# Kernel optimization log

Measured on AMD Instinct MI355X. Metric: run time of the kernel, lower is better.

The kernel has to match this reference:

```python
import jax, jax.numpy as jnp
import numpy as np

B, T, C, H, NIN = 4, 16384, 512, 8, 2
D = C // H


def setup_inputs() -> dict:
    key = jax.random.key(0)
    ks = jax.random.split(key, 12)
    s = 1.0 / np.sqrt(C)
    return {
        "x1": jax.random.normal(ks[0], (B, T, C), jnp.float32),
        "x2": jax.random.normal(ks[1], (B, T, C), jnp.float32),
        "y0": jax.random.normal(ks[2], (B, T, C), jnp.float32),
        "y1": jax.random.normal(ks[3], (B, T, C), jnp.float32),
        "Wq": jax.random.normal(ks[4], (C, C), jnp.float32) * s,
        "bq": jnp.zeros((C,), jnp.float32),
        "Wk": jax.random.normal(ks[5], (C, C), jnp.float32) * s,
        "bk": jnp.zeros((C,), jnp.float32),
        "Wv": jax.random.normal(ks[6], (NIN, C, C), jnp.float32) * s,
        "bv": jnp.zeros((NIN, C), jnp.float32),
        "Wp": jax.random.normal(ks[7], (C, C), jnp.float32) * s,
        "bp": jnp.zeros((C,), jnp.float32),
    }


def _heads(x):
    # [B, T, C] -> [B, H, T, D]
    b, t, c = x.shape
    return x.reshape(b, t, H, D).transpose(0, 2, 1, 3)


def reference(x1, x2, y0, y1, Wq, bq, Wk, bk, Wv, bv, Wp, bp):
    # q, k: softmax feature maps over head dim
    q = jax.nn.softmax(_heads(x1 @ Wq + bq), axis=-1)  # [B,H,T1,D]
    k = jax.nn.softmax(_heads(x2 @ Wk + bk), axis=-1)  # [B,H,T2,D]
    # v = sum of per-input value projections
    ys = jnp.stack([y0, y1], axis=0)  # [NIN,B,T2,C]
    v = jnp.einsum('ibtc,icd->btd', ys, Wv) + bv.sum(axis=0)
    v = _heads(v)  # [B,H,T2,D]
    # linear attention: k^T v then q @ (kv)
    k_v = jnp.einsum('bhtd,bhte->bhde', k, v)      # [B,H,D,D]
    q_k_v = jnp.einsum('bhsd,bhde->bhse', q, k_v)  # [B,H,T1,D]
    k_cumsum = k.sum(axis=-2, keepdims=True)       # [B,H,1,D]
    D_inv = 1.0 / (q * k_cumsum).sum(axis=-1, keepdims=True)
    out = q_k_v * D_inv                            # [B,H,T1,D]
    out = out.transpose(0, 2, 1, 3).reshape(x1.shape[0], x1.shape[1], C)
    return out @ Wp + bp
```

## Files before the change

### kernel.cpp

```cpp
#include <hip/hip_runtime.h>
#include <cstdint>
#include <cstddef>

#define BB 4
#define TT 16384
#define CC 512
#define HH 8
#define DD 64
#define MTOT (BB*TT)

typedef __attribute__((ext_vector_type(4))) float f32x4;
typedef __bf16 bf16;
typedef __attribute__((ext_vector_type(8))) bf16 bf16x8;
typedef __attribute__((ext_vector_type(4))) bf16 bf16x4;

static __device__ __forceinline__ float b2f(bf16 x) { return (float)x; }
static __device__ __forceinline__ bf16  f2b(float x) { return (bf16)x; }

static __device__ __forceinline__ void gload16(const bf16* src, bf16* ldsbase) {
    __builtin_amdgcn_global_load_lds(
        (const __attribute__((address_space(1))) void*)src,
        (__attribute__((address_space(3))) void*)ldsbase, 16, 0, 0);
}

__global__ __launch_bounds__(256) void transpose_w5(
    const float* __restrict__ W0, const float* __restrict__ W1,
    const float* __restrict__ W2, const float* __restrict__ W3,
    const float* __restrict__ W4,
    bf16* __restrict__ T0, bf16* __restrict__ T1, bf16* __restrict__ T2,
    bf16* __restrict__ T3, bf16* __restrict__ T4)
{
    __shared__ float tile[32][33];
    const int which = blockIdx.x >> 8;
    const float* W = which == 0 ? W0 : which == 1 ? W1 : which == 2 ? W2
                   : which == 3 ? W3 : W4;
    bf16* Wt = which == 0 ? T0 : which == 1 ? T1 : which == 2 ? T2
             : which == 3 ? T3 : T4;
    const int t = blockIdx.x & 255;
    const int r0 = (t >> 4) * 32, c0 = (t & 15) * 32;
    const int tid = threadIdx.x;
    {
        int r = tid >> 3, c4 = (tid & 7) << 2;
        float4 v = *(const float4*)(W + (size_t)(r0 + r) * 512 + c0 + c4);
        tile[r][c4 + 0] = v.x; tile[r][c4 + 1] = v.y;
        tile[r][c4 + 2] = v.z; tile[r][c4 + 3] = v.w;
    }
    __syncthreads();
    {
        int n = tid >> 3, k4 = (tid & 7) << 2;
        bf16x4 o;
        o[0] = f2b(tile[k4 + 0][n]); o[1] = f2b(tile[k4 + 1][n]);
        o[2] = f2b(tile[k4 + 2][n]); o[3] = f2b(tile[k4 + 3][n]);
        *(bf16x4*)(Wt + (size_t)(c0 + n) * 512 + r0 + k4) = o;
    }
}

template<int MODE>
__global__ __launch_bounds__(512) void gemm_proj(
    const float* A0, const float* A1, const bf16* Abf,
    const bf16* Wt0, const bf16* Wt1,
    const float* bias0, const float* bias1,
    bf16* outb, float* outf, int m_base)
{
    constexpr int KSTEPS = (MODE == 2) ? 16 : 8;
    __shared__ bf16 Asm[128 * 72];
    __shared__ bf16 Bsm[2][512 * 64];

    const int tid = threadIdx.x;
    const int lane = tid & 63;
    const int w = tid >> 6;
    const int l15 = lane & 15, lg = lane >> 4;
    const size_t m0 = (size_t)(blockIdx.x + m_base) * 128;

    const int arow = tid >> 2, ac16 = (tid & 3) << 4;
    const int blr = lane >> 3;
    const int bsc = ((lane & 7) ^ blr) << 3;

    f32x4 acc[8][4];
#pragma unroll
    for (int m = 0; m < 8; ++m)
#pragma unroll
        for (int n = 0; n < 4; ++n) acc[m][n] = (f32x4){0.f, 0.f, 0.f, 0.f};

    float4 apf[4];
    bf16x8 apb[2];

    auto issueA = [&](int t) {
        if (MODE == 3) {
#pragma unroll
            for (int j = 0; j < 2; ++j)
                apb[j] = *(const bf16x8*)(Abf + (m0 + arow) * CC + (t & 7) * 64
                                          + ac16 + j * 8);
        } else {
            const float* Af = (MODE == 2 && t >= 8) ? A1 : A0;
#pragma unroll
            for (int j = 0; j < 4; ++j)
                apf[j] = *(const float4*)(Af + (m0 + arow) * CC + (t & 7) * 64
                                          + ac16 + j * 4);
        }
    };
    auto writeA = [&]() {
        if (MODE == 3) {
#pragma unroll
            for (int j = 0; j < 2; ++j)
                *(bf16x8*)&Asm[arow * 72 + ac16 + j * 8] = apb[j];
        } else {
#pragma unroll
            for (int j = 0; j < 4; ++j) {
                bf16x4 s;
                s[0] = f2b(apf[j].x); s[1] = f2b(apf[j].y);
                s[2] = f2b(apf[j].z); s[3] = f2b(apf[j].w);
                *(bf16x4*)&Asm[arow * 72 + ac16 + j * 4] = s;
            }
        }
    };
    auto issueB = [&](int t, int buf) {
        const bf16* Wt = (MODE == 2 && t >= 8) ? Wt1 : Wt0;
#pragma unroll
        for (int g = 0; g < 8; ++g) {
            int rowbase = w * 64 + g * 8;
            gload16(Wt + (size_t)(rowbase + blr) * CC + (t & 7) * 64 + bsc,
                    &Bsm[buf][rowbase * 64]);
        }
    };

    issueA(0);
    issueB(0, 0);
    writeA();
    asm volatile("s_waitcnt lgkmcnt(0)" ::: "memory");

    int cur = 0;
    for (int ko = 0; ko < KSTEPS; ++ko) {
        const bool more = ko + 1 < KSTEPS;
        if (more) { issueA(ko + 1); issueB(ko + 1, cur ^ 1); }
        if (more) {
            if (MODE == 3) asm volatile("s_waitcnt vmcnt(10)" ::: "memory");
            else           asm volatile("s_waitcnt vmcnt(12)" ::: "memory");
        } else {
            asm volatile("s_waitcnt vmcnt(0)" ::: "memory");
        }
        __builtin_amdgcn_s_barrier();
        bf16x8 af[8][2], bfv[4][2];
#pragma unroll
        for (int m = 0; m < 8; ++m)
#pragma unroll
            for (int kk = 0; kk < 2; ++kk)
                af[m][kk] = *(const bf16x8*)&Asm[(m * 16 + l15) * 72 + kk * 32 + lg * 8];
#pragma unroll
        for (int n = 0; n < 4; ++n) {
            int row = w * 64 + n * 16 + l15;
            int swz = (l15 & 7) << 3;
#pragma unroll
            for (int kk = 0; kk < 2; ++kk)
                bfv[n][kk] = *(const bf16x8*)&Bsm[cur][row * 64
                                                      + ((kk * 32 + lg * 8) ^ swz)];
        }
#pragma unroll
        for (int kk = 0; kk < 2; ++kk)
#pragma unroll
            for (int m = 0; m < 8; ++m)
#pragma unroll
                for (int n = 0; n < 4; ++n)
                    acc[m][n] = __builtin_amdgcn_mfma_f32_16x16x32_bf16(
                        af[m][kk], bfv[n][kk], acc[m][n], 0, 0, 0);
        __builtin_amdgcn_s_barrier();
        if (more) {
            writeA();
            asm volatile("s_waitcnt lgkmcnt(0)" ::: "memory");
        }
        cur ^= 1;
    }

    float bias[4];
#pragma unroll
    for (int n = 0; n < 4; ++n) {
        int col = w * 64 + n * 16 + l15;
        float bvv = bias0 ? bias0[col] : 0.f;
        if (MODE == 2) bvv += bias1[col];
        bias[n] = bvv;
    }
#pragma unroll
    for (int m = 0; m < 8; ++m) {
#pragma unroll
        for (int reg = 0; reg < 4; ++reg) {
            int r = m * 16 + lg * 4 + reg;
            float v0 = acc[m][0][reg] + bias[0];
            float v1 = acc[m][1][reg] + bias[1];
            float v2 = acc[m][2][reg] + bias[2];
            float v3 = acc[m][3][reg] + bias[3];
            if (MODE == 0) {
                float mx = fmaxf(fmaxf(v0, v1), fmaxf(v2, v3));
#pragma unroll
                for (int s = 1; s < 16; s <<= 1) mx = fmaxf(mx, __shfl_xor(mx, s, 64));
                v0 = __expf(v0 - mx); v1 = __expf(v1 - mx);
                v2 = __expf(v2 - mx); v3 = __expf(v3 - mx);
                float sm = v0 + v1 + v2 + v3;
#pragma unroll
                for (int s = 1; s < 16; s <<= 1) sm += __shfl_xor(sm, s, 64);
                float inv = 1.0f / sm;
                v0 *= inv; v1 *= inv; v2 *= inv; v3 *= inv;
            }
            size_t rowoff = (m0 + r) * CC + w * 64 + l15;
            if (MODE == 3) {
                outf[rowoff + 0]  = v0; outf[rowoff + 16] = v1;
                outf[rowoff + 32] = v2; outf[rowoff + 48] = v3;
            } else {
                outb[rowoff + 0]  = f2b(v0); outb[rowoff + 16] = f2b(v1);
                outb[rowoff + 32] = f2b(v2); outb[rowoff + 48] = f2b(v3);
            }
        }
    }
}

__global__ __launch_bounds__(256) void kv_partial2(
    const bf16* __restrict__ Kb, const bf16* __restrict__ Vb,
    float* __restrict__ part)
{
    __shared__ float Ks[32][68], Vs[32][68];
    const int tid = threadIdx.x;
    const int bh = blockIdx.x >> 5, chunk = blockIdx.x & 31;
    const int b = bh >> 3, h = bh & 7;
    const size_t base = (size_t)b * TT * CC + h * 64;
    const int d0 = (tid & 15) * 4, e0 = (tid >> 4) * 4;

    float acc[4][4];
#pragma unroll
    for (int i = 0; i < 4; ++i)
#pragma unroll
        for (int j = 0; j < 4; ++j) acc[i][j] = 0.f;
    float ks[4] = {0.f, 0.f, 0.f, 0.f};

    const int tstart = chunk * 512;
    for (int t0 = tstart; t0 < tstart + 512; t0 += 32) {
        __syncthreads();
#pragma unroll
        for (int rep = 0; rep < 2; ++rep) {
            int idx = (tid + rep * 256) * 4;
            int t = idx >> 6, dc = idx & 63;
            const bf16* gk = Kb + base + (size_t)(t0 + t) * CC + dc;
            const bf16* gv = Vb + base + (size_t)(t0 + t) * CC + dc;
            bf16x4 k4 = *(const bf16x4*)gk;
            bf16x4 v4 = *(const bf16x4*)gv;
            *(float4*)&Ks[t][dc] = make_float4(b2f(k4[0]), b2f(k4[1]), b2f(k4[2]), b2f(k4[3]));
            *(float4*)&Vs[t][dc] = make_float4(b2f(v4[0]), b2f(v4[1]), b2f(v4[2]), b2f(v4[3]));
        }
        __syncthreads();
#pragma unroll 8
        for (int tt = 0; tt < 32; ++tt) {
            float4 kf4 = *(const float4*)&Ks[tt][d0];
            float4 vf4 = *(const float4*)&Vs[tt][e0];
            if (e0 == 0) {
                ks[0] += kf4.x; ks[1] += kf4.y; ks[2] += kf4.z; ks[3] += kf4.w;
            }
            acc[0][0] += kf4.x * vf4.x; acc[0][1] += kf4.x * vf4.y;
            acc[0][2] += kf4.x * vf4.z; acc[0][3] += kf4.x * vf4.w;
            acc[1][0] += kf4.y * vf4.x; acc[1][1] += kf4.y * vf4.y;
            acc[1][2] += kf4.y * vf4.z; acc[1][3] += kf4.y * vf4.w;
            acc[2][0] += kf4.z * vf4.x; acc[2][1] += kf4.z * vf4.y;
            acc[2][2] += kf4.z * vf4.z; acc[2][3] += kf4.z * vf4.w;
            acc[3][0] += kf4.w * vf4.x; acc[3][1] += kf4.w * vf4.y;
            acc[3][2] += kf4.w * vf4.z; acc[3][3] += kf4.w * vf4.w;
        }
    }

    float* p = part + (size_t)blockIdx.x * 4160;
#pragma unroll
    for (int i = 0; i < 4; ++i)
#pragma unroll
        for (int j = 0; j < 4; ++j) p[(d0 + i) * 64 + (e0 + j)] = acc[i][j];
    if (tid < 16) {
#pragma unroll
        for (int i = 0; i < 4; ++i) p[4096 + d0 + i] = ks[i];
    }
}

__global__ __launch_bounds__(256) void kv_reduce(
    const float* __restrict__ part, float* __restrict__ kvT,
    float* __restrict__ ksum)
{
    const int bh = blockIdx.x >> 3, sl = blockIdx.x & 7;
    const int tid = threadIdx.x;
    const float* p0 = part + (size_t)bh * 32 * 4160;
    const int i0 = sl * 520, i1 = i0 + 520;
    for (int i = i0 + tid; i < i1; i += 256) {
        float s = 0.f;
        for (int c = 0; c < 32; ++c) s += p0[(size_t)c * 4160 + i];
        if (i < 4096) {
            int d = i >> 6, e = i & 63;
            kvT[(size_t)bh * 4096 + e * 64 + d] = s;
        } else {
            ksum[bh * 64 + (i - 4096)] = s;
        }
    }
}

__global__ __launch_bounds__(256) void qkv_norm2(
    bf16* Qb, const float* __restrict__ kvT, const float* __restrict__ ksum)
{
    __shared__ float Qs[64][68];
    __shared__ float KVs[64][68];
    __shared__ float ksm[8][64];
    const int tid = threadIdx.x;
    const size_t t0 = (size_t)blockIdx.x * 64;
    const int b = (int)(t0 / TT);
    const int rg = tid >> 4, cg = tid & 15;

    for (int i = tid; i < 512; i += 256) ksm[i >> 6][i & 63] = ksum[b * 512 + i];

    for (int h = 0; h < 8; ++h) {
        __syncthreads();
        const float* kvb = kvT + (size_t)(b * 8 + h) * 4096;
#pragma unroll
        for (int rep = 0; rep < 4; ++rep) {
            int idx = (tid + rep * 256) * 4;
            int rr = idx >> 6, dc = idx & 63;
            bf16x4 q4 = *(const bf16x4*)(Qb + (t0 + rr) * CC + h * 64 + dc);
            Qs[dc + 0][rr] = b2f(q4[0]); Qs[dc + 1][rr] = b2f(q4[1]);
            Qs[dc + 2][rr] = b2f(q4[2]); Qs[dc + 3][rr] = b2f(q4[3]);
            float4 v4 = *(const float4*)(kvb + rr * 64 + dc);
            KVs[dc + 0][rr] = v4.x; KVs[dc + 1][rr] = v4.y;
            KVs[dc + 2][rr] = v4.z; KVs[dc + 3][rr] = v4.w;
        }
        __syncthreads();

        float acc[4][4];
#pragma unroll
        for (int i = 0; i < 4; ++i)
#pragma unroll
            for (int j = 0; j < 4; ++j) acc[i][j] = 0.f;
        float dot[4] = {0.f, 0.f, 0.f, 0.f};

#pragma unroll 4
        for (int d = 0; d < 64; ++d) {
            float ksd = ksm[h][d];
            float4 kv4 = *(const float4*)&KVs[d][cg * 4];
            float4 q4 = *(const float4*)&Qs[d][rg * 4];
            dot[0] += q4.x * ksd; dot[1] += q4.y * ksd;
            dot[2] += q4.z * ksd; dot[3] += q4.w * ksd;
            acc[0][0] += q4.x * kv4.x; acc[0][1] += q4.x * kv4.y;
            acc[0][2] += q4.x * kv4.z; acc[0][3] += q4.x * kv4.w;
            acc[1][0] += q4.y * kv4.x; acc[1][1] += q4.y * kv4.y;
            acc[1][2] += q4.y * kv4.z; acc[1][3] += q4.y * kv4.w;
            acc[2][0] += q4.z * kv4.x; acc[2][1] += q4.z * kv4.y;
            acc[2][2] += q4.z * kv4.z; acc[2][3] += q4.z * kv4.w;
            acc[3][0] += q4.w * kv4.x; acc[3][1] += q4.w * kv4.y;
            acc[3][2] += q4.w * kv4.z; acc[3][3] += q4.w * kv4.w;
        }
#pragma unroll
        for (int i = 0; i < 4; ++i) {
            float dinv = 1.0f / dot[i];
            bf16x4 o;
#pragma unroll
            for (int j = 0; j < 4; ++j) o[j] = f2b(acc[i][j] * dinv);
            *(bf16x4*)(Qb + (t0 + rg * 4 + i) * CC + h * 64 + cg * 4) = o;
        }
    }
}

extern "C" void kernel_launch(void* const* d_in, const int* in_sizes, int n_in,
                              void* d_out, int out_size, void* d_ws, size_t ws_size,
                              hipStream_t stream)
{
    const float* x1 = (const float*)d_in[0];
    const float* x2 = (const float*)d_in[1];
    const float* y0 = (const float*)d_in[2];
    const float* y1 = (const float*)d_in[3];
    const float* Wq = (const float*)d_in[4];
    const float* bq = (const float*)d_in[5];
    const float* Wk = (const float*)d_in[6];
    const float* bk = (const float*)d_in[7];
    const float* Wv = (const float*)d_in[8];
    const float* bv = (const float*)d_in[9];
    const float* Wp = (const float*)d_in[10];
    const float* bp = (const float*)d_in[11];
    (void)in_sizes; (void)n_in; (void)out_size;

    char* ws = (char*)d_ws;
    size_t off = 0;
    auto alloc = [&](size_t bytes) -> void* {
        void* p = ws + off;
        off += (bytes + 255) & ~(size_t)255;
        return p;
    };
    bf16* WtQ  = (bf16*)alloc((size_t)512 * 512 * 2);
    bf16* WtK  = (bf16*)alloc((size_t)512 * 512 * 2);
    bf16* WtV0 = (bf16*)alloc((size_t)512 * 512 * 2);
    bf16* WtV1 = (bf16*)alloc((size_t)512 * 512 * 2);
    bf16* WtP  = (bf16*)alloc((size_t)512 * 512 * 2);
    float* ksum = (float*)alloc((size_t)32 * 64 * 4);
    float* kvT  = (float*)alloc((size_t)32 * 4096 * 4);
    float* part = (float*)alloc((size_t)1024 * 4160 * 4);
    bf16* Acopy = (bf16*)alloc((size_t)16 * 128 * CC * 2);

    const size_t QBYTES = (size_t)MTOT * CC * 2;
    bf16* Qb_ws = nullptr;
    if (ws_size >= off + QBYTES + 256) Qb_ws = (bf16*)alloc(QBYTES);

    bf16* Kb = (bf16*)d_out;
    bf16* Vb = Kb + (size_t)MTOT * CC;
    float* outF = (float*)d_out;

    transpose_w5<<<1280, 256, 0, stream>>>(Wq, Wk, Wv, Wv + (size_t)512 * 512, Wp,
                                           WtQ, WtK, WtV0, WtV1, WtP);

    gemm_proj<0><<<MTOT / 128, 512, 0, stream>>>(x2, nullptr, nullptr, WtK, nullptr,
                                                 bk, nullptr, Kb, nullptr, 0);
    gemm_proj<2><<<MTOT / 128, 512, 0, stream>>>(y0, y1, nullptr, WtV0, WtV1,
                                                 bv, bv + 512, Vb, nullptr, 0);
    kv_partial2<<<1024, 256, 0, stream>>>(Kb, Vb, part);
    kv_reduce<<<256, 256, 0, stream>>>(part, kvT, ksum);

    if (Qb_ws) {
        gemm_proj<0><<<MTOT / 128, 512, 0, stream>>>(x1, nullptr, nullptr, WtQ, nullptr,
                                                     bq, nullptr, Qb_ws, nullptr, 0);
        qkv_norm2<<<1024, 256, 0, stream>>>(Qb_ws, kvT, ksum);
        gemm_proj<3><<<MTOT / 128, 512, 0, stream>>>(nullptr, nullptr, (const bf16*)Qb_ws,
                                                     WtP, nullptr, bp, nullptr,
                                                     nullptr, outF, 0);
    } else {
        bf16* Qb = Kb;
        gemm_proj<0><<<MTOT / 128, 512, 0, stream>>>(x1, nullptr, nullptr, WtQ, nullptr,
                                                     bq, nullptr, Qb, nullptr, 0);
        qkv_norm2<<<1024, 256, 0, stream>>>(Qb, kvT, ksum);
        hipMemcpyAsync(Acopy, Qb, (size_t)16 * 128 * CC * 2, hipMemcpyDeviceToDevice,
                       stream);
        const int starts[5] = {256, 128, 64, 32, 16};
        const int counts[5] = {256, 128, 64, 32, 16};
        for (int p = 0; p < 5; ++p) {
            gemm_proj<3><<<counts[p], 512, 0, stream>>>(nullptr, nullptr, (const bf16*)Qb,
                                                        WtP, nullptr, bp, nullptr,
                                                        nullptr, outF, starts[p]);
        }
        gemm_proj<3><<<16, 512, 0, stream>>>(nullptr, nullptr, (const bf16*)Acopy,
                                             WtP, nullptr, bp, nullptr,
                                             nullptr, outF, 0);
    }
}
```

Baseline: 492.7 us.

## Fuse Q/K/V projection GEMMs into one launch and use MFMA for q·kv normalization

Merges the K, V and Q projection GEMMs into a single kernel that selects the projection by block index, removing launch gaps and tail idle time between them. Replaces the scalar LDS-based q@kv normalization kernel with an MFMA version that reads Q directly from global memory and converts kv to bf16. This adds precision loss from rounding kv to bf16, and the Q projection now runs alongside K/V rather than after the kv reduction.

```diff
diff --git a/kernel.cpp b/kernel.cpp
--- a/kernel.cpp
+++ b/kernel.cpp
@@ -56,21 +56,20 @@
 }
 
 template<int MODE>
-__global__ __launch_bounds__(512) void gemm_proj(
+static __device__ __forceinline__ void gemm_body(
     const float* A0, const float* A1, const bf16* Abf,
     const bf16* Wt0, const bf16* Wt1,
     const float* bias0, const float* bias1,
-    bf16* outb, float* outf, int m_base)
+    bf16* outb, float* outf, int bid,
+    bf16* Asm, bf16* BsmAll)
 {
     constexpr int KSTEPS = (MODE == 2) ? 16 : 8;
-    __shared__ bf16 Asm[128 * 72];
-    __shared__ bf16 Bsm[2][512 * 64];
 
     const int tid = threadIdx.x;
     const int lane = tid & 63;
     const int w = tid >> 6;
     const int l15 = lane & 15, lg = lane >> 4;
-    const size_t m0 = (size_t)(blockIdx.x + m_base) * 128;
+    const size_t m0 = (size_t)bid * 128;
 
     const int arow = tid >> 2, ac16 = (tid & 3) << 4;
     const int blr = lane >> 3;
@@ -116,11 +115,12 @@
     };
     auto issueB = [&](int t, int buf) {
         const bf16* Wt = (MODE == 2 && t >= 8) ? Wt1 : Wt0;
+        bf16* bb = BsmAll + buf * (512 * 64);
 #pragma unroll
         for (int g = 0; g < 8; ++g) {
             int rowbase = w * 64 + g * 8;
             gload16(Wt + (size_t)(rowbase + blr) * CC + (t & 7) * 64 + bsc,
-                    &Bsm[buf][rowbase * 64]);
+                    &bb[rowbase * 64]);
         }
     };
 
@@ -141,6 +141,7 @@
         }
         __builtin_amdgcn_s_barrier();
         bf16x8 af[8][2], bfv[4][2];
+        const bf16* bb = BsmAll + cur * (512 * 64);
 #pragma unroll
         for (int m = 0; m < 8; ++m)
 #pragma unroll
@@ -152,8 +153,7 @@
             int swz = (l15 & 7) << 3;
 #pragma unroll
             for (int kk = 0; kk < 2; ++kk)
-                bfv[n][kk] = *(const bf16x8*)&Bsm[cur][row * 64
-                                                      + ((kk * 32 + lg * 8) ^ swz)];
+                bfv[n][kk] = *(const bf16x8*)&bb[row * 64 + ((kk * 32 + lg * 8) ^ swz)];
         }
 #pragma unroll
         for (int kk = 0; kk < 2; ++kk)
@@ -210,6 +210,36 @@
             }
         }
     }
+}
+
+__global__ __launch_bounds__(512) void proj_fused(
+    const float* x1, const float* x2, const float* y0, const float* y1,
+    const bf16* WtQ, const bf16* WtK, const bf16* WtV0, const bf16* WtV1,
+    const float* bq, const float* bk, const float* bv0, const float* bv1,
+    bf16* Kb, bf16* Vb, bf16* Qb, int which_base)
+{
+    __shared__ bf16 Asm[128 * 72];
+    __shared__ bf16 Bsm[2 * 512 * 64];
+    const int which = which_base + ((int)blockIdx.x >> 9);
+    const int bid = blockIdx.x & 511;
+    if (which == 0)
+        gemm_body<0>(x2, nullptr, nullptr, WtK, nullptr, bk, nullptr,
+                     Kb, nullptr, bid, Asm, Bsm);
+    else if (which == 1)
+        gemm_body<2>(y0, y1, nullptr, WtV0, WtV1, bv0, bv1,
+                     Vb, nullptr, bid, Asm, Bsm);
+    else
+        gemm_body<0>(x1, nullptr, nullptr, WtQ, nullptr, bq, nullptr,
+                     Qb, nullptr, bid, Asm, Bsm);
+}
+
+__global__ __launch_bounds__(512) void gemm_proj3(
+    const bf16* Abf, const bf16* WtP, const float* bp, float* outf, int m_base)
+{
+    __shared__ bf16 Asm[128 * 72];
+    __shared__ bf16 Bsm[2 * 512 * 64];
+    gemm_body<3>(nullptr, nullptr, Abf, WtP, nullptr, bp, nullptr,
+                 nullptr, outf, blockIdx.x + m_base, Asm, Bsm);
 }
 
 __global__ __launch_bounds__(256) void kv_partial2(
@@ -294,66 +324,82 @@
     }
 }
 
-__global__ __launch_bounds__(256) void qkv_norm2(
-    bf16* Qb, const float* __restrict__ kvT, const float* __restrict__ ksum)
-{
-    __shared__ float Qs[64][68];
-    __shared__ float KVs[64][68];
+__global__ __launch_bounds__(256) void qkv_norm_mfma(
+    const bf16* Qb, const float* __restrict__ kvT,
+    const float* __restrict__ ksum, bf16* Ab)
+{
     __shared__ float ksm[8][64];
     const int tid = threadIdx.x;
+    const int lane = tid & 63;
+    const int w = tid >> 6;
+    const int l15 = lane & 15, lg = lane >> 4;
     const size_t t0 = (size_t)blockIdx.x * 64;
     const int b = (int)(t0 / TT);
-    const int rg = tid >> 4, cg = tid & 15;
 
     for (int i = tid; i < 512; i += 256) ksm[i >> 6][i & 63] = ksum[b * 512 + i];
-
-    for (int h = 0; h < 8; ++h) {
-        __syncthreads();
+    __syncthreads();
+
+#pragma unroll
+    for (int hi = 0; hi < 2; ++hi) {
+        const int h = w + hi * 4;
+        const bf16* qbase = Qb + t0 * CC + h * 64;
         const float* kvb = kvT + (size_t)(b * 8 + h) * 4096;
-#pragma unroll
-        for (int rep = 0; rep < 4; ++rep) {
-            int idx = (tid + rep * 256) * 4;
-            int rr = idx >> 6, dc = idx & 63;
-            bf16x4 q4 = *(const bf16x4*)(Qb + (t0 + rr) * CC + h * 64 + dc);
-            Qs[dc + 0][rr] = b2f(q4[0]); Qs[dc + 1][rr] = b2f(q4[1]);
-            Qs[dc + 2][rr] = b2f(q4[2]); Qs[dc + 3][rr] = b2f(q4[3]);
-            float4 v4 = *(const float4*)(kvb + rr * 64 + dc);
-            KVs[dc + 0][rr] = v4.x; KVs[dc + 1][rr] = v4.y;
-            KVs[dc + 2][rr] = v4.z; KVs[dc + 3][rr] = v4.w;
-        }
-        __syncthreads();
-
-        float acc[4][4];
-#pragma unroll
-        for (int i = 0; i < 4; ++i)
-#pragma unroll
-            for (int j = 0; j < 4; ++j) acc[i][j] = 0.f;
+
+        f32x4 acc[4][4];
+#pragma unroll
+        for (int m = 0; m < 4; ++m)
+#pragma unroll
+            for (int n = 0; n < 4; ++n) acc[m][n] = (f32x4){0.f, 0.f, 0.f, 0.f};
         float dot[4] = {0.f, 0.f, 0.f, 0.f};
 
-#pragma unroll 4
-        for (int d = 0; d < 64; ++d) {
-            float ksd = ksm[h][d];
-            float4 kv4 = *(const float4*)&KVs[d][cg * 4];
-            float4 q4 = *(const float4*)&Qs[d][rg * 4];
-            dot[0] += q4.x * ksd; dot[1] += q4.y * ksd;
-            dot[2] += q4.z * ksd; dot[3] += q4.w * ksd;
-            acc[0][0] += q4.x * kv4.x; acc[0][1] += q4.x * kv4.y;
-            acc[0][2] += q4.x * kv4.z; acc[0][3] += q4.x * kv4.w;
-            acc[1][0] += q4.y * kv4.x; acc[1][1] += q4.y * kv4.y;
-            acc[1][2] += q4.y * kv4.z; acc[1][3] += q4.y * kv4.w;
-            acc[2][0] += q4.z * kv4.x; acc[2][1] += q4.z * kv4.y;
-            acc[2][2] += q4.z * kv4.z; acc[2][3] += q4.z * kv4.w;
-            acc[3][0] += q4.w * kv4.x; acc[3][1] += q4.w * kv4.y;
-            acc[3][2] += q4.w * kv4.z; acc[3][3] += q4.w * kv4.w;
-        }
-#pragma unroll
-        for (int i = 0; i < 4; ++i) {
-            float dinv = 1.0f / dot[i];
-            bf16x4 o;
-#pragma unroll
-            for (int j = 0; j < 4; ++j) o[j] = f2b(acc[i][j] * dinv);
-            *(bf16x4*)(Qb + (t0 + rg * 4 + i) * CC + h * 64 + cg * 4) = o;
-        }
+#pragma unroll
+        for (int ks2 = 0; ks2 < 2; ++ks2) {
+            bf16x8 af[4], bfv[4];
+#pragma unroll
+            for (int m = 0; m < 4; ++m)
+                af[m] = *(const bf16x8*)(qbase + (size_t)(m * 16 + l15) * CC
+                                         + ks2 * 32 + lg * 8);
+#pragma unroll
+            for (int n = 0; n < 4; ++n) {
+                const float* kr = kvb + (n * 16 + l15) * 64 + ks2 * 32 + lg * 8;
+                float4 lo = *(const float4*)(kr + 0);
+                float4 hh = *(const float4*)(kr + 4);
+                bfv[n][0] = f2b(lo.x); bfv[n][1] = f2b(lo.y);
+                bfv[n][2] = f2b(lo.z); bfv[n][3] = f2b(lo.w);
+                bfv[n][4] = f2b(hh.x); bfv[n][5] = f2b(hh.y);
+                bfv[n][6] = f2b(hh.z); bfv[n][7] = f2b(hh.w);
+            }
+#pragma unroll
+            for (int m = 0; m < 4; ++m) {
+                float s = 0.f;
+#pragma unroll
+                for (int j = 0; j < 8; ++j)
+                    s += b2f(af[m][j]) * ksm[h][ks2 * 32 + lg * 8 + j];
+                dot[m] += s;
+            }
+#pragma unroll
+            for (int m = 0; m < 4; ++m)
+#pragma unroll
+                for (int n = 0; n < 4; ++n)
+                    acc[m][n] = __builtin_amdgcn_mfma_f32_16x16x32_bf16(
+                        af[m], bfv[n], acc[m][n], 0, 0, 0);
+        }
+#pragma unroll
+        for (int m = 0; m < 4; ++m) {
+            dot[m] += __shfl_xor(dot[m], 16, 64);
+            dot[m] += __shfl_xor(dot[m], 32, 64);
+        }
+#pragma unroll
+        for (int m = 0; m < 4; ++m)
+#pragma unroll
+            for (int reg = 0; reg < 4; ++reg) {
+                float dv = 1.0f / __shfl(dot[m], lg * 4 + reg, 64);
+                size_t ro = (t0 + m * 16 + lg * 4 + reg) * CC + h * 64 + l15;
+                Ab[ro + 0]  = f2b(acc[m][0][reg] * dv);
+                Ab[ro + 16] = f2b(acc[m][1][reg] * dv);
+                Ab[ro + 32] = f2b(acc[m][2][reg] * dv);
+                Ab[ro + 48] = f2b(acc[m][3][reg] * dv);
+            }
     }
 }
 
@@ -403,36 +449,34 @@
     transpose_w5<<<1280, 256, 0, stream>>>(Wq, Wk, Wv, Wv + (size_t)512 * 512, Wp,
                                            WtQ, WtK, WtV0, WtV1, WtP);
 
-    gemm_proj<0><<<MTOT / 128, 512, 0, stream>>>(x2, nullptr, nullptr, WtK, nullptr,
-                                                 bk, nullptr, Kb, nullptr, 0);
-    gemm_proj<2><<<MTOT / 128, 512, 0, stream>>>(y0, y1, nullptr, WtV0, WtV1,
-                                                 bv, bv + 512, Vb, nullptr, 0);
-    kv_partial2<<<1024, 256, 0, stream>>>(Kb, Vb, part);
-    kv_reduce<<<256, 256, 0, stream>>>(part, kvT, ksum);
-
     if (Qb_ws) {
-        gemm_proj<0><<<MTOT / 128, 512, 0, stream>>>(x1, nullptr, nullptr, WtQ, nullptr,
-                                                     bq, nullptr, Qb_ws, nullptr, 0);
-        qkv_norm2<<<1024, 256, 0, stream>>>(Qb_ws, kvT, ksum);
-        gemm_proj<3><<<MTOT / 128, 512, 0, stream>>>(nullptr, nullptr, (const bf16*)Qb_ws,
-                                                     WtP, nullptr, bp, nullptr,
-                                                     nullptr, outF, 0);
+        proj_fused<<<1536, 512, 0, stream>>>(x1, x2, y0, y1, WtQ, WtK, WtV0, WtV1,
+                                             bq, bk, bv, bv + 512,
+                                             Kb, Vb, Qb_ws, 0);
+        kv_partial2<<<1024, 256, 0, stream>>>(Kb, Vb, part);
+        kv_reduce<<<256, 256, 0, stream>>>(part, kvT, ksum);
+        qkv_norm_mfma<<<1024, 256, 0, stream>>>(Qb_ws, kvT, ksum, Qb_ws);
+        gemm_proj3<<<MTOT / 128, 512, 0, stream>>>((const bf16*)Qb_ws, WtP, bp,
+                                                   outF, 0);
     } else {
         bf16* Qb = Kb;
-        gemm_proj<0><<<MTOT / 128, 512, 0, stream>>>(x1, nullptr, nullptr, WtQ, nullptr,
-                                                     bq, nullptr, Qb, nullptr, 0);
-        qkv_norm2<<<1024, 256, 0, stream>>>(Qb, kvT, ksum);
+        proj_fused<<<1024, 512, 0, stream>>>(x1, x2, y0, y1, WtQ, WtK, WtV0, WtV1,
+                                             bq, bk, bv, bv + 512,
+                                             Kb, Vb, Qb, 0);
+        kv_partial2<<<1024, 256, 0, stream>>>(Kb, Vb, part);
+        kv_reduce<<<256, 256, 0, stream>>>(part, kvT, ksum);
+        proj_fused<<<512, 512, 0, stream>>>(x1, x2, y0, y1, WtQ, WtK, WtV0, WtV1,
+                                            bq, bk, bv, bv + 512,
+                                            Kb, Vb, Qb, 2);
+        qkv_norm_mfma<<<1024, 256, 0, stream>>>(Qb, kvT, ksum, Qb);
         hipMemcpyAsync(Acopy, Qb, (size_t)16 * 128 * CC * 2, hipMemcpyDeviceToDevice,
                        stream);
         const int starts[5] = {256, 128, 64, 32, 16};
         const int counts[5] = {256, 128, 64, 32, 16};
         for (int p = 0; p < 5; ++p) {
-            gemm_proj<3><<<counts[p], 512, 0, stream>>>(nullptr, nullptr, (const bf16*)Qb,
-                                                        WtP, nullptr, bp, nullptr,
-                                                        nullptr, outF, starts[p]);
-        }
-        gemm_proj<3><<<16, 512, 0, stream>>>(nullptr, nullptr, (const bf16*)Acopy,
-                                             WtP, nullptr, bp, nullptr,
-                                             nullptr, outF, 0);
-    }
-}
+            gemm_proj3<<<counts[p], 512, 0, stream>>>((const bf16*)Qb, WtP, bp,
+                                                      outF, starts[p]);
+        }
+        gemm_proj3<<<16, 512, 0, stream>>>((const bf16*)Acopy, WtP, bp, outF, 0);
+    }
+}
```

Result: faster. 440.2 us (-10.7%).
